# Kernel tuning notes

Hardware: AMD Instinct MI355X
Metric: run time of the kernel (lower is better)

Reference implementation:

```python
import jax, jax.numpy as jnp
import numpy as np

TANH_SCALAR = 10.0  # taug in IrEne eq. 1 (close_to_one setting)

N_NODES = 2**21 - 1   # complete binary tree, depth D=21
N_LEAVES = 2**20
NUM_FEATURES = 64


def setup_inputs() -> dict:
    key = jax.random.key(0)
    k1, k2, k3, k4 = jax.random.split(key, 4)
    features = jax.random.normal(k1, (N_NODES, NUM_FEATURES), dtype=jnp.float32)
    leaf_energy = jax.random.uniform(k2, (N_LEAVES,), dtype=jnp.float32)
    W = jax.random.normal(k3, (NUM_FEATURES, 1), dtype=jnp.float32) * 0.1
    b = jax.random.normal(k4, (1,), dtype=jnp.float32) * 0.1
    return {"features": features, "leaf_energy": leaf_energy, "W": W, "b": b}


def reference(features, leaf_energy, W, b):
    """Batched equivalent of RecursiveTreeComputation (close_to_one, end2end).

    Tree layout: complete binary tree in level order; node i's parent is (i-1)//2.
    Level d occupies indices [2^d - 1, 2^{d+1} - 1). Leaves are the last level.
    parent_energy = sum_children score(child) * child_energy,
    score(f) = 1 + tanh(f @ W + b) / tanh_scalar.
    Returns predicted energy for every node, shape [N].
    """
    N, F = features.shape
    D = int(np.log2(N + 1))  # number of levels (static)

    # One fused pass over all nodes: Linear(F,1) + tanh + affine (WeightingModel).
    scores = 1.0 + jnp.tanh(features @ W + b)[:, 0] / TANH_SCALAR  # [N]

    leaf_start = 2 ** (D - 1) - 1
    energy = jnp.zeros((N,), dtype=features.dtype).at[leaf_start:].set(leaf_energy)

    # Level-wise bottom-up accumulation; consecutive child pairs share a parent.
    for d in range(D - 1, 0, -1):
        start, end = 2 ** d - 1, 2 ** (d + 1) - 1          # children at level d
        contrib = scores[start:end] * energy[start:end]      # weighted child energies
        parent_vals = contrib.reshape(-1, 2).sum(axis=1)     # sum sibling pairs
        pstart = 2 ** (d - 1) - 1                             # parents at level d-1
        energy = energy.at[pstart:start].set(energy[pstart:start] + parent_vals)
    return energy
```

## Files before the change

kernel.cpp:

```cpp
#include <hip/hip_runtime.h>
#include <cmath>

#define N_NODES_C   ((1 << 21) - 1)
#define N_LEAVES_C  (1 << 20)
#define LEAF_START  (N_LEAVES_C - 1)
#define NFEAT       64

__device__ __forceinline__ float score_fn(float dot, float bias) {
    return 1.0f + tanhf(dot + bias) * 0.1f;
}

__global__ __launch_bounds__(256) void scores_kernel(
        const float* __restrict__ features,
        const float* __restrict__ W,
        const float* __restrict__ b,
        float* __restrict__ scores) {
    const int q = threadIdx.x & 15;
    const float4 w4 = ((const float4*)W)[q];
    const float bias = b[0];
    const int group0 = (blockIdx.x * 256 + threadIdx.x) >> 4;
    const int stride = (gridDim.x * 256) >> 4;
    for (int node = group0; node < N_NODES_C; node += stride) {
        const float4 f = ((const float4*)(features + (size_t)node * NFEAT))[q];
        float v = f.x * w4.x + f.y * w4.y + f.z * w4.z + f.w * w4.w;
        v += __shfl_xor(v, 1);
        v += __shfl_xor(v, 2);
        v += __shfl_xor(v, 4);
        v += __shfl_xor(v, 8);
        if (q == 0) scores[node] = score_fn(v, bias);
    }
}

__global__ __launch_bounds__(256) void stage1_kernel(
        const float* __restrict__ scores,
        const float* __restrict__ leaf_energy,
        float* __restrict__ out) {
    __shared__ float buf[2][4096];
    const int blk = blockIdx.x;
    const int tid = threadIdx.x;
    const int leaf_off = blk * 4096;

    for (int i = tid; i < 4096; i += 256) {
        const int g = LEAF_START + leaf_off + i;
        const float e = leaf_energy[leaf_off + i];
        out[g] = e;
        buf[0][i] = scores[g] * e;
    }
    __syncthreads();

    int p = 0;
    for (int pd = 19; pd >= 8; --pd) {
        const int m = 1 << (pd - 8);
        const int base = (1 << pd) - 1 + blk * m;
        for (int j = tid; j < m; j += 256) {
            const float val = buf[p][2 * j] + buf[p][2 * j + 1];
            out[base + j] = val;
            buf[1 - p][j] = scores[base + j] * val;
        }
        p ^= 1;
        __syncthreads();
    }
}

__global__ __launch_bounds__(256) void stage2_kernel(
        const float* __restrict__ scores,
        float* __restrict__ out) {
    __shared__ float buf[2][256];
    const int tid = threadIdx.x;
    buf[0][tid] = scores[255 + tid] * out[255 + tid];
    __syncthreads();
    int p = 0;
    for (int pd = 7; pd >= 0; --pd) {
        const int m = 1 << pd;
        const int base = m - 1;
        if (tid < m) {
            const float val = buf[p][2 * tid] + buf[p][2 * tid + 1];
            out[base + tid] = val;
            buf[1 - p][tid] = scores[base + tid] * val;
        }
        p ^= 1;
        __syncthreads();
    }
}

extern "C" void kernel_launch(void* const* d_in, const int* in_sizes, int n_in,
                              void* d_out, int out_size, void* d_ws, size_t ws_size,
                              hipStream_t stream) {
    const float* features    = (const float*)d_in[0];
    const float* leaf_energy = (const float*)d_in[1];
    const float* W           = (const float*)d_in[2];
    const float* b           = (const float*)d_in[3];
    float* out    = (float*)d_out;
    float* scores = (float*)d_ws;

    scores_kernel<<<32768, 256, 0, stream>>>(features, W, b, scores);
    stage1_kernel<<<256, 256, 0, stream>>>(scores, leaf_energy, out);
    stage2_kernel<<<1, 256, 0, stream>>>(scores, out);
}
```

Before: 691.8 us.

## Use one thread per node for scores and split the tree reduction across more blocks

The scores kernel now gives each thread a whole 64-float feature row and loops over 16 float4 loads, replacing the 16-lane group with shuffle reduction. This removes the shuffles but makes each lane's loads strided by 256 bytes, so global reads are uncoalesced. The tree reduction now uses 1024 blocks of 1024 leaves instead of 256 blocks of 4096 leaves, which raises parallelism in stage 1. The single-block stage 2 in exchange has to handle ten levels instead of eight.

```diff
diff --git a/kernel.cpp b/kernel.cpp
--- a/kernel.cpp
+++ b/kernel.cpp
@@ -6,41 +6,35 @@
 #define LEAF_START  (N_LEAVES_C - 1)
 #define NFEAT       64
 
-__device__ __forceinline__ float score_fn(float dot, float bias) {
-    return 1.0f + tanhf(dot + bias) * 0.1f;
-}
-
 __global__ __launch_bounds__(256) void scores_kernel(
         const float* __restrict__ features,
         const float* __restrict__ W,
         const float* __restrict__ b,
         float* __restrict__ scores) {
-    const int q = threadIdx.x & 15;
-    const float4 w4 = ((const float4*)W)[q];
-    const float bias = b[0];
-    const int group0 = (blockIdx.x * 256 + threadIdx.x) >> 4;
-    const int stride = (gridDim.x * 256) >> 4;
-    for (int node = group0; node < N_NODES_C; node += stride) {
-        const float4 f = ((const float4*)(features + (size_t)node * NFEAT))[q];
-        float v = f.x * w4.x + f.y * w4.y + f.z * w4.z + f.w * w4.w;
-        v += __shfl_xor(v, 1);
-        v += __shfl_xor(v, 2);
-        v += __shfl_xor(v, 4);
-        v += __shfl_xor(v, 8);
-        if (q == 0) scores[node] = score_fn(v, bias);
+    const int node = blockIdx.x * 256 + threadIdx.x;
+    if (node >= N_NODES_C) return;
+    const float4* __restrict__ fp = (const float4*)(features + (size_t)node * NFEAT);
+    const float4* __restrict__ wp = (const float4*)W;
+    float acc = 0.0f;
+#pragma unroll
+    for (int k = 0; k < 16; ++k) {
+        const float4 f = fp[k];
+        const float4 w = wp[k];
+        acc += f.x * w.x + f.y * w.y + f.z * w.z + f.w * w.w;
     }
+    scores[node] = 1.0f + tanhf(acc + b[0]) * 0.1f;
 }
 
 __global__ __launch_bounds__(256) void stage1_kernel(
         const float* __restrict__ scores,
         const float* __restrict__ leaf_energy,
         float* __restrict__ out) {
-    __shared__ float buf[2][4096];
+    __shared__ float buf[2][1024];
     const int blk = blockIdx.x;
     const int tid = threadIdx.x;
-    const int leaf_off = blk * 4096;
+    const int leaf_off = blk * 1024;
 
-    for (int i = tid; i < 4096; i += 256) {
+    for (int i = tid; i < 1024; i += 256) {
         const int g = LEAF_START + leaf_off + i;
         const float e = leaf_energy[leaf_off + i];
         out[g] = e;
@@ -49,8 +43,8 @@
     __syncthreads();
 
     int p = 0;
-    for (int pd = 19; pd >= 8; --pd) {
-        const int m = 1 << (pd - 8);
+    for (int pd = 19; pd >= 10; --pd) {
+        const int m = 1 << (pd - 10);
         const int base = (1 << pd) - 1 + blk * m;
         for (int j = tid; j < m; j += 256) {
             const float val = buf[p][2 * j] + buf[p][2 * j + 1];
@@ -65,18 +59,19 @@
 __global__ __launch_bounds__(256) void stage2_kernel(
         const float* __restrict__ scores,
         float* __restrict__ out) {
-    __shared__ float buf[2][256];
+    __shared__ float buf[2][1024];
     const int tid = threadIdx.x;
-    buf[0][tid] = scores[255 + tid] * out[255 + tid];
+    for (int i = tid; i < 1024; i += 256)
+        buf[0][i] = scores[1023 + i] * out[1023 + i];
     __syncthreads();
     int p = 0;
-    for (int pd = 7; pd >= 0; --pd) {
+    for (int pd = 9; pd >= 0; --pd) {
         const int m = 1 << pd;
         const int base = m - 1;
-        if (tid < m) {
-            const float val = buf[p][2 * tid] + buf[p][2 * tid + 1];
-            out[base + tid] = val;
-            buf[1 - p][tid] = scores[base + tid] * val;
+        for (int j = tid; j < m; j += 256) {
+            const float val = buf[p][2 * j] + buf[p][2 * j + 1];
+            out[base + j] = val;
+            buf[1 - p][j] = scores[base + j] * val;
         }
         p ^= 1;
         __syncthreads();
@@ -93,7 +88,7 @@
     float* out    = (float*)d_out;
     float* scores = (float*)d_ws;
 
-    scores_kernel<<<32768, 256, 0, stream>>>(features, W, b, scores);
-    stage1_kernel<<<256, 256, 0, stream>>>(scores, leaf_energy, out);
+    scores_kernel<<<(N_NODES_C + 255) / 256, 256, 0, stream>>>(features, W, b, scores);
+    stage1_kernel<<<1024, 256, 0, stream>>>(scores, leaf_energy, out);
     stage2_kernel<<<1, 256, 0, stream>>>(scores, out);
 }
```

Measured after the change: 699.5 us. Within noise of the previous version (+1.1%).
